# Kernel optimization log

Measured on AMD Instinct MI355X. Metric: run time of the kernel, lower is better.

Reference implementation:

```python
import jax, jax.numpy as jnp
import numpy as np

WINDOW_SIZE = 11
SIGMA = 1.5
C1 = 0.01 ** 2
C2 = 0.03 ** 2


def _gaussian_window(channels):
    coords = jnp.arange(WINDOW_SIZE, dtype=jnp.float32) - WINDOW_SIZE // 2
    g = jnp.exp(-coords ** 2 / (2.0 * SIGMA ** 2))
    g = g / g.sum()
    w2d = g[:, None] * g[None, :]                      # [K, K]
    # depthwise kernel: [out_ch=C, in_ch/groups=1, K, K]
    return jnp.broadcast_to(w2d[None, None], (channels, 1, WINDOW_SIZE, WINDOW_SIZE))


def _depthwise_conv(x, window):
    # x: [B, C, H, W]; grouped conv with feature_group_count = C, SAME padding
    C = x.shape[1]
    pad = WINDOW_SIZE // 2
    return jax.lax.conv_general_dilated(
        x, window,
        window_strides=(1, 1),
        padding=((pad, pad), (pad, pad)),
        dimension_numbers=("NCHW", "OIHW", "NCHW"),
        feature_group_count=C,
    )


def setup_inputs() -> dict:
    key = jax.random.key(0)
    k1, k2 = jax.random.split(key)
    shape = (16, 3, 512, 512)
    pred = jax.random.uniform(k1, shape, dtype=jnp.float32)
    target = jax.random.uniform(k2, shape, dtype=jnp.float32)
    return {"pred": pred, "target": target}


def reference(pred, target):
    C = pred.shape[1]
    window = _gaussian_window(C)
    mu_p = _depthwise_conv(pred, window)
    mu_t = _depthwise_conv(target, window)
    mu_p_sq = mu_p ** 2
    mu_t_sq = mu_t ** 2
    mu_cross = mu_p * mu_t
    sigma_p_sq = _depthwise_conv(pred ** 2, window) - mu_p_sq
    sigma_t_sq = _depthwise_conv(target ** 2, window) - mu_t_sq
    sigma_cross = _depthwise_conv(pred * target, window) - mu_cross
    ssim_map = ((2.0 * mu_cross + C1) * (2.0 * sigma_cross + C2)) / (
        (mu_p_sq + mu_t_sq + C1) * (sigma_p_sq + sigma_t_sq + C2)
    )
    return 1.0 - ssim_map.mean()
```

## Files before the change

kernel.cpp:

```cpp
#include <hip/hip_runtime.h>

#define HH 512
#define WW 512
#define NPLANE 48
#define BY 128
#define CHK 16
#define NCH (BY / CHK)
#define SLOTS 40
#define KS 11

typedef __attribute__((ext_vector_type(8))) short short8;
typedef __attribute__((ext_vector_type(4))) float floatx4;
typedef __attribute__((ext_vector_type(2))) float float2v;
typedef __attribute__((ext_vector_type(2))) __bf16 bf16x2v;

__device__ inline unsigned pk2bf_rne(float a, float b) {
    union { float f; unsigned u; } ua, ub;
    ua.f = a; ub.f = b;
    unsigned lo = (ua.u + 0x7FFFu + ((ua.u >> 16) & 1u)) >> 16;
    unsigned hi = (ub.u + 0x7FFFu + ((ub.u >> 16) & 1u)) >> 16;
    return lo | (hi << 16);
}

__device__ inline unsigned pkbf(float a, float b) {
    float2v f = {a, b};
    bf16x2v v = __builtin_convertvector(f, bf16x2v);
    return __builtin_bit_cast(unsigned, v);
}

struct Raw { float4 p0, p1, t0, t1; };

__global__ __launch_bounds__(256, 4) void ssim_kernel(
    const float* __restrict__ pred, const float* __restrict__ target,
    float* __restrict__ ws_sum)
{
    __shared__ __align__(16) short ring[4][5][16][SLOTS];
    __shared__ float red[4];

    const int tid = threadIdx.x;
    const int wv = tid >> 6;
    const int lane = tid & 63;
    const int m = lane & 15;
    const int quad = lane >> 4;

    float wsum = 0.f;
#pragma unroll
    for (int k = 0; k < KS; ++k) {
        float d = (float)(k - 5);
        wsum += __expf(-d * d * (1.0f / 4.5f));
    }
    const float invs = 1.0f / wsum;

    short8 Wf;
    {
        union { short8 v; unsigned u[4]; } W;
#pragma unroll
        for (int jj = 0; jj < 4; ++jj) {
            float v0, v1;
            {
                int idx = quad * 8 + 2 * jj - m - 3;
                float d = (float)(idx - 5);
                v0 = (idx >= 0 && idx < KS) ? __expf(-d * d * (1.0f / 4.5f)) * invs : 0.f;
            }
            {
                int idx = quad * 8 + 2 * jj + 1 - m - 3;
                float d = (float)(idx - 5);
                v1 = (idx >= 0 && idx < KS) ? __expf(-d * d * (1.0f / 4.5f)) * invs : 0.f;
            }
            W.u[jj] = pk2bf_rne(v0, v1);
        }
        Wf = W.v;
    }

    const size_t poff = (size_t)blockIdx.z * HH * WW;
    const float* __restrict__ pp = pred + poff;
    const float* __restrict__ tp = target + poff;
    const int X0 = blockIdx.x * 64 + wv * 16;
    const int rawX = X0 - 8;
    const int Y0 = blockIdx.y * BY;

    const float C1 = 1.0e-4f;
    const float C2 = 9.0e-4f;
    float lsum = 0.f;
    const floatx4 z = {0.f, 0.f, 0.f, 0.f};

    auto load_raw = [&](int k) -> Raw {
        Raw r;
        r.p0 = make_float4(0, 0, 0, 0); r.p1 = make_float4(0, 0, 0, 0);
        r.t0 = make_float4(0, 0, 0, 0); r.t1 = make_float4(0, 0, 0, 0);
        const int row = Y0 + CHK * k - 8 + m;
        if ((unsigned)row < (unsigned)HH) {
            const float* pr = pp + (size_t)row * WW;
            const float* tr = tp + (size_t)row * WW;
            const int c0 = rawX + quad * 8;
            if ((unsigned)c0 < (unsigned)WW) {
                r.p0 = *(const float4*)(pr + c0);
                r.t0 = *(const float4*)(tr + c0);
            }
            if ((unsigned)(c0 + 4) < (unsigned)WW) {
                r.p1 = *(const float4*)(pr + c0 + 4);
                r.t1 = *(const float4*)(tr + c0 + 4);
            }
        }
        return r;
    };

    auto h_step = [&](const Raw& r, int sb) {
        const float p[8] = {r.p0.x, r.p0.y, r.p0.z, r.p0.w,
                            r.p1.x, r.p1.y, r.p1.z, r.p1.w};
        const float t[8] = {r.t0.x, r.t0.y, r.t0.z, r.t0.w,
                            r.t1.x, r.t1.y, r.t1.z, r.t1.w};
        union { short8 v; unsigned u[4]; } Fp, Ft, Fpp, Ftt, Fpt;
#pragma unroll
        for (int jj = 0; jj < 4; ++jj) {
            const float a0 = p[2 * jj], a1 = p[2 * jj + 1];
            const float b0 = t[2 * jj], b1 = t[2 * jj + 1];
            Fp.u[jj]  = pkbf(a0, a1);
            Ft.u[jj]  = pkbf(b0, b1);
            Fpp.u[jj] = pkbf(a0 * a0, a1 * a1);
            Ftt.u[jj] = pkbf(b0 * b0, b1 * b1);
            Fpt.u[jj] = pkbf(a0 * b0, a1 * b1);
        }
        floatx4 Dp  = __builtin_amdgcn_mfma_f32_16x16x32_bf16(Fp.v,  Wf, z, 0, 0, 0);
        floatx4 Dt  = __builtin_amdgcn_mfma_f32_16x16x32_bf16(Ft.v,  Wf, z, 0, 0, 0);
        floatx4 Dpp = __builtin_amdgcn_mfma_f32_16x16x32_bf16(Fpp.v, Wf, z, 0, 0, 0);
        floatx4 Dtt = __builtin_amdgcn_mfma_f32_16x16x32_bf16(Ftt.v, Wf, z, 0, 0, 0);
        floatx4 Dpt = __builtin_amdgcn_mfma_f32_16x16x32_bf16(Fpt.v, Wf, z, 0, 0, 0);
        int slot = sb + quad * 4;
        if (slot >= SLOTS) slot -= SLOTS;
        uint2 v;
        v.x = pkbf(Dp[0], Dp[1]);   v.y = pkbf(Dp[2], Dp[3]);
        *(uint2*)&ring[wv][0][m][slot] = v;
        v.x = pkbf(Dt[0], Dt[1]);   v.y = pkbf(Dt[2], Dt[3]);
        *(uint2*)&ring[wv][1][m][slot] = v;
        v.x = pkbf(Dpp[0], Dpp[1]); v.y = pkbf(Dpp[2], Dpp[3]);
        *(uint2*)&ring[wv][2][m][slot] = v;
        v.x = pkbf(Dtt[0], Dtt[1]); v.y = pkbf(Dtt[2], Dtt[3]);
        *(uint2*)&ring[wv][3][m][slot] = v;
        v.x = pkbf(Dpt[0], Dpt[1]); v.y = pkbf(Dpt[2], Dpt[3]);
        *(uint2*)&ring[wv][4][m][slot] = v;
    };

    Raw A = load_raw(0);
    Raw B = load_raw(1);
    Raw C = load_raw(2);
    h_step(A, (0 * CHK + SLOTS - 8) % SLOTS);
    h_step(B, (1 * CHK + SLOTS - 8) % SLOTS);
    int hb = (2 * CHK + SLOTS - 8) % SLOTS;
    int vb = SLOTS - 8;
#pragma unroll 1
    for (int i = 0; i < NCH; ++i) {
        int sq = vb + quad * 8;
        if (sq >= SLOTS) sq -= SLOTS;
        const short8 Bp  = *(const short8*)&ring[wv][0][m][sq];
        const short8 Bt  = *(const short8*)&ring[wv][1][m][sq];
        const short8 Bpp = *(const short8*)&ring[wv][2][m][sq];
        const short8 Btt = *(const short8*)&ring[wv][3][m][sq];
        const short8 Bpt = *(const short8*)&ring[wv][4][m][sq];
        vb += CHK; if (vb >= SLOTS) vb -= SLOTS;

        if (i + 2 <= NCH) {
            h_step(C, hb);
            hb += CHK; if (hb >= SLOTS) hb -= SLOTS;
        }
        if (i + 3 <= NCH) C = load_raw(i + 3);

        floatx4 Mp  = __builtin_amdgcn_mfma_f32_16x16x32_bf16(Wf, Bp,  z, 0, 0, 0);
        floatx4 Mt  = __builtin_amdgcn_mfma_f32_16x16x32_bf16(Wf, Bt,  z, 0, 0, 0);
        floatx4 Mpp = __builtin_amdgcn_mfma_f32_16x16x32_bf16(Wf, Bpp, z, 0, 0, 0);
        floatx4 Mtt = __builtin_amdgcn_mfma_f32_16x16x32_bf16(Wf, Btt, z, 0, 0, 0);
        floatx4 Mpt = __builtin_amdgcn_mfma_f32_16x16x32_bf16(Wf, Bpt, z, 0, 0, 0);
#pragma unroll
        for (int r = 0; r < 4; ++r) {
            const float mup = Mp[r], mut = Mt[r];
            const float mupsq = mup * mup, mutsq = mut * mut, mucr = mup * mut;
            const float sp2 = Mpp[r] - mupsq;
            const float st2 = Mtt[r] - mutsq;
            const float scr = Mpt[r] - mucr;
            const float n1 = 2.f * mucr + C1;
            const float n2 = 2.f * scr + C2;
            const float d1 = mupsq + mutsq + C1;
            const float d2 = sp2 + st2 + C2;
            lsum += __fdividef(n1 * n2, d1 * d2);
        }
    }

#pragma unroll
    for (int off = 32; off > 0; off >>= 1) lsum += __shfl_down(lsum, off, 64);
    if (lane == 0) red[wv] = lsum;
    __syncthreads();
    if (tid == 0) {
        atomicAdd(ws_sum, red[0] + red[1] + red[2] + red[3]);
    }
}

__global__ void finalize_kernel(const float* __restrict__ ws_sum,
                                float* __restrict__ out) {
    out[0] = 1.0f - ws_sum[0] * (1.0f / 12582912.0f);
}

extern "C" void kernel_launch(void* const* d_in, const int* in_sizes, int n_in,
                              void* d_out, int out_size, void* d_ws, size_t ws_size,
                              hipStream_t stream) {
    const float* pred = (const float*)d_in[0];
    const float* target = (const float*)d_in[1];
    float* out = (float*)d_out;
    float* ws = (float*)d_ws;

    hipMemsetAsync(ws, 0, sizeof(float), stream);
    dim3 grid(WW / 64, HH / BY, NPLANE);
    ssim_kernel<<<grid, 256, 0, stream>>>(pred, target, ws);
    finalize_kernel<<<1, 1, 0, stream>>>(ws, out);
}
```

Before: 141.4 us.

## Merge squared-sum convolutions, halve row tile, fuse finalize into last block

The p² and t² channels are combined into one p²+t² channel before the separable Gaussian MFMA convolution, since SSIM only needs their sum. This cuts the horizontal and vertical MFMAs, LDS ring writes and reads from five streams to four. The row tile shrinks from 128 to 64, giving twice as many blocks, with launch bounds raised to 8 waves-per-EU and the chunk loop fully unrolled. The separate finalize kernel is replaced by a last-block-done counter that writes the result. The trade-offs are more halo rows reloaded per output, bf16 rounding of the summed squares, and register pressure under the tighter launch bound.

```diff
diff --git a/kernel.cpp b/kernel.cpp
--- a/kernel.cpp
+++ b/kernel.cpp
@@ -3,11 +3,12 @@
 #define HH 512
 #define WW 512
 #define NPLANE 48
-#define BY 128
+#define BY 64
 #define CHK 16
 #define NCH (BY / CHK)
 #define SLOTS 40
 #define KS 11
+#define NBLK ((WW / 64) * (HH / BY) * NPLANE)
 
 typedef __attribute__((ext_vector_type(8))) short short8;
 typedef __attribute__((ext_vector_type(4))) float floatx4;
@@ -30,12 +31,11 @@
 
 struct Raw { float4 p0, p1, t0, t1; };
 
-__global__ __launch_bounds__(256, 4) void ssim_kernel(
+__global__ __launch_bounds__(256, 8) void ssim_kernel(
     const float* __restrict__ pred, const float* __restrict__ target,
-    float* __restrict__ ws_sum)
+    float* __restrict__ ws, float* __restrict__ out)
 {
-    __shared__ __align__(16) short ring[4][5][16][SLOTS];
-    __shared__ float red[4];
+    __shared__ __align__(16) short ring[4][4][16][SLOTS];
 
     const int tid = threadIdx.x;
     const int wv = tid >> 6;
@@ -110,21 +110,19 @@
                             r.p1.x, r.p1.y, r.p1.z, r.p1.w};
         const float t[8] = {r.t0.x, r.t0.y, r.t0.z, r.t0.w,
                             r.t1.x, r.t1.y, r.t1.z, r.t1.w};
-        union { short8 v; unsigned u[4]; } Fp, Ft, Fpp, Ftt, Fpt;
+        union { short8 v; unsigned u[4]; } Fp, Ft, Fq, Fpt;
 #pragma unroll
         for (int jj = 0; jj < 4; ++jj) {
             const float a0 = p[2 * jj], a1 = p[2 * jj + 1];
             const float b0 = t[2 * jj], b1 = t[2 * jj + 1];
             Fp.u[jj]  = pkbf(a0, a1);
             Ft.u[jj]  = pkbf(b0, b1);
-            Fpp.u[jj] = pkbf(a0 * a0, a1 * a1);
-            Ftt.u[jj] = pkbf(b0 * b0, b1 * b1);
+            Fq.u[jj]  = pkbf(fmaf(a0, a0, b0 * b0), fmaf(a1, a1, b1 * b1));
             Fpt.u[jj] = pkbf(a0 * b0, a1 * b1);
         }
         floatx4 Dp  = __builtin_amdgcn_mfma_f32_16x16x32_bf16(Fp.v,  Wf, z, 0, 0, 0);
         floatx4 Dt  = __builtin_amdgcn_mfma_f32_16x16x32_bf16(Ft.v,  Wf, z, 0, 0, 0);
-        floatx4 Dpp = __builtin_amdgcn_mfma_f32_16x16x32_bf16(Fpp.v, Wf, z, 0, 0, 0);
-        floatx4 Dtt = __builtin_amdgcn_mfma_f32_16x16x32_bf16(Ftt.v, Wf, z, 0, 0, 0);
+        floatx4 Dq  = __builtin_amdgcn_mfma_f32_16x16x32_bf16(Fq.v,  Wf, z, 0, 0, 0);
         floatx4 Dpt = __builtin_amdgcn_mfma_f32_16x16x32_bf16(Fpt.v, Wf, z, 0, 0, 0);
         int slot = sb + quad * 4;
         if (slot >= SLOTS) slot -= SLOTS;
@@ -133,12 +131,10 @@
         *(uint2*)&ring[wv][0][m][slot] = v;
         v.x = pkbf(Dt[0], Dt[1]);   v.y = pkbf(Dt[2], Dt[3]);
         *(uint2*)&ring[wv][1][m][slot] = v;
-        v.x = pkbf(Dpp[0], Dpp[1]); v.y = pkbf(Dpp[2], Dpp[3]);
+        v.x = pkbf(Dq[0], Dq[1]);   v.y = pkbf(Dq[2], Dq[3]);
         *(uint2*)&ring[wv][2][m][slot] = v;
-        v.x = pkbf(Dtt[0], Dtt[1]); v.y = pkbf(Dtt[2], Dtt[3]);
+        v.x = pkbf(Dpt[0], Dpt[1]); v.y = pkbf(Dpt[2], Dpt[3]);
         *(uint2*)&ring[wv][3][m][slot] = v;
-        v.x = pkbf(Dpt[0], Dpt[1]); v.y = pkbf(Dpt[2], Dpt[3]);
-        *(uint2*)&ring[wv][4][m][slot] = v;
     };
 
     Raw A = load_raw(0);
@@ -148,15 +144,14 @@
     h_step(B, (1 * CHK + SLOTS - 8) % SLOTS);
     int hb = (2 * CHK + SLOTS - 8) % SLOTS;
     int vb = SLOTS - 8;
-#pragma unroll 1
+#pragma unroll
     for (int i = 0; i < NCH; ++i) {
         int sq = vb + quad * 8;
         if (sq >= SLOTS) sq -= SLOTS;
         const short8 Bp  = *(const short8*)&ring[wv][0][m][sq];
         const short8 Bt  = *(const short8*)&ring[wv][1][m][sq];
-        const short8 Bpp = *(const short8*)&ring[wv][2][m][sq];
-        const short8 Btt = *(const short8*)&ring[wv][3][m][sq];
-        const short8 Bpt = *(const short8*)&ring[wv][4][m][sq];
+        const short8 Bq  = *(const short8*)&ring[wv][2][m][sq];
+        const short8 Bpt = *(const short8*)&ring[wv][3][m][sq];
         vb += CHK; if (vb >= SLOTS) vb -= SLOTS;
 
         if (i + 2 <= NCH) {
@@ -167,36 +162,39 @@
 
         floatx4 Mp  = __builtin_amdgcn_mfma_f32_16x16x32_bf16(Wf, Bp,  z, 0, 0, 0);
         floatx4 Mt  = __builtin_amdgcn_mfma_f32_16x16x32_bf16(Wf, Bt,  z, 0, 0, 0);
-        floatx4 Mpp = __builtin_amdgcn_mfma_f32_16x16x32_bf16(Wf, Bpp, z, 0, 0, 0);
-        floatx4 Mtt = __builtin_amdgcn_mfma_f32_16x16x32_bf16(Wf, Btt, z, 0, 0, 0);
+        floatx4 Mq  = __builtin_amdgcn_mfma_f32_16x16x32_bf16(Wf, Bq,  z, 0, 0, 0);
         floatx4 Mpt = __builtin_amdgcn_mfma_f32_16x16x32_bf16(Wf, Bpt, z, 0, 0, 0);
 #pragma unroll
         for (int r = 0; r < 4; ++r) {
             const float mup = Mp[r], mut = Mt[r];
             const float mupsq = mup * mup, mutsq = mut * mut, mucr = mup * mut;
-            const float sp2 = Mpp[r] - mupsq;
-            const float st2 = Mtt[r] - mutsq;
             const float scr = Mpt[r] - mucr;
             const float n1 = 2.f * mucr + C1;
             const float n2 = 2.f * scr + C2;
             const float d1 = mupsq + mutsq + C1;
-            const float d2 = sp2 + st2 + C2;
+            const float d2 = (Mq[r] - mupsq - mutsq) + C2;
             lsum += __fdividef(n1 * n2, d1 * d2);
         }
     }
 
 #pragma unroll
     for (int off = 32; off > 0; off >>= 1) lsum += __shfl_down(lsum, off, 64);
-    if (lane == 0) red[wv] = lsum;
+    if (lane == 0) *(float*)&ring[wv][0][0][0] = lsum;
     __syncthreads();
     if (tid == 0) {
-        atomicAdd(ws_sum, red[0] + red[1] + red[2] + red[3]);
-    }
-}
-
-__global__ void finalize_kernel(const float* __restrict__ ws_sum,
-                                float* __restrict__ out) {
-    out[0] = 1.0f - ws_sum[0] * (1.0f / 12582912.0f);
+        float bsum = *(const float*)&ring[0][0][0][0]
+                   + *(const float*)&ring[1][0][0][0]
+                   + *(const float*)&ring[2][0][0][0]
+                   + *(const float*)&ring[3][0][0][0];
+        atomicAdd(&ws[0], bsum);
+        __threadfence();
+        unsigned old = atomicAdd((unsigned int*)&ws[1], 1u);
+        if (old == (unsigned)(NBLK - 1)) {
+            __threadfence();
+            float total = atomicAdd(&ws[0], 0.0f);
+            out[0] = 1.0f - total * (1.0f / 12582912.0f);
+        }
+    }
 }
 
 extern "C" void kernel_launch(void* const* d_in, const int* in_sizes, int n_in,
@@ -207,8 +205,7 @@
     float* out = (float*)d_out;
     float* ws = (float*)d_ws;
 
-    hipMemsetAsync(ws, 0, sizeof(float), stream);
+    hipMemsetAsync(ws, 0, 2 * sizeof(float), stream);
     dim3 grid(WW / 64, HH / BY, NPLANE);
-    ssim_kernel<<<grid, 256, 0, stream>>>(pred, target, ws);
-    finalize_kernel<<<1, 1, 0, stream>>>(ws, out);
-}
+    ssim_kernel<<<grid, 256, 0, stream>>>(pred, target, ws, out);
+}
```

After: 279.5 us. +97.7%, slower.
